# Optimization experiments

Hardware: AMD Instinct MI355X
Metric: run time of the kernel (lower is better)

Reference implementation:

```python
import jax, jax.numpy as jnp
import numpy as np

D_MODEL = 512
N_HEADS = 8
EDGE_FEAT_DIM = 4
NUM_GRAPHS = 64
NODES_PER_GRAPH = 128
N_NODES = NUM_GRAPHS * NODES_PER_GRAPH          # 8192
EDGES_PER_GRAPH = 4096                           # avg degree 32
N_EDGES = NUM_GRAPHS * EDGES_PER_GRAPH           # 262144


def setup_inputs() -> dict:
    key = jax.random.key(0)
    ks = jax.random.split(key, 12)
    s = 0.02
    x = jax.random.normal(ks[0], (N_NODES, D_MODEL), jnp.float32)
    # edges constrained within their graph (block-diagonal structure)
    g_of_e = jnp.arange(N_EDGES, dtype=jnp.int32) // EDGES_PER_GRAPH
    src = g_of_e * NODES_PER_GRAPH + jax.random.randint(ks[1], (N_EDGES,), 0, NODES_PER_GRAPH, jnp.int32)
    dst = g_of_e * NODES_PER_GRAPH + jax.random.randint(ks[2], (N_EDGES,), 0, NODES_PER_GRAPH, jnp.int32)
    edge_index = jnp.stack([src, dst]).astype(jnp.int32)
    edge_attr = jax.random.normal(ks[3], (N_EDGES, EDGE_FEAT_DIM), jnp.float32)
    batch = jnp.repeat(jnp.arange(NUM_GRAPHS, dtype=jnp.int32), NODES_PER_GRAPH)
    # projection weights (in,out) convention: y = x @ W + b
    Wq = jax.random.normal(ks[4], (D_MODEL, D_MODEL), jnp.float32) * s
    Wk = jax.random.normal(ks[5], (D_MODEL, D_MODEL), jnp.float32) * s
    Wv = jax.random.normal(ks[6], (D_MODEL, D_MODEL), jnp.float32) * s
    Wo = jax.random.normal(ks[7], (D_MODEL, D_MODEL), jnp.float32) * s
    bq = jnp.zeros((D_MODEL,), jnp.float32)
    bk = jnp.zeros((D_MODEL,), jnp.float32)
    bv = jnp.zeros((D_MODEL,), jnp.float32)
    bo = jnp.zeros((D_MODEL,), jnp.float32)
    # edge bias MLP: edge_feat_dim -> d_model -> n_heads
    W1 = jax.random.normal(ks[8], (EDGE_FEAT_DIM, D_MODEL), jnp.float32) * s
    b1 = jnp.zeros((D_MODEL,), jnp.float32)
    W2 = jax.random.normal(ks[9], (D_MODEL, N_HEADS), jnp.float32) * s
    b2 = jnp.zeros((N_HEADS,), jnp.float32)
    return {"x": x, "edge_index": edge_index, "edge_attr": edge_attr, "batch": batch,
            "n_g": NODES_PER_GRAPH,
            "Wq": Wq, "bq": bq, "Wk": Wk, "bk": bk, "Wv": Wv, "bv": bv,
            "Wo": Wo, "bo": bo, "W1": W1, "b1": b1, "W2": W2, "b2": b2}


def reference(x, edge_index, edge_attr, batch, n_g, Wq, bq, Wk, bk, Wv, bv, Wo, bo, W1, b1, W2, b2):
    # batch is contiguous equal-size blocks of n_g nodes per graph, so the
    # per-graph Python loop of the original collapses to a batched (G, n_g)
    # block-diagonal attention. Dropout is identity (eval / p used only in train).
    N, d_model = x.shape
    H = W2.shape[1]
    d_k = d_model // H
    G = N // n_g
    scale = 1.0 / float(np.sqrt(d_k))

    Q = (x @ Wq + bq).reshape(G, n_g, H, d_k)
    K = (x @ Wk + bk).reshape(G, n_g, H, d_k)
    V = (x @ Wv + bv).reshape(G, n_g, H, d_k)

    # (G, i, j, h) dense per-graph scores
    scores = jnp.einsum('gihd,gjhd->gijh', Q, K) * scale

    # edge bias: MLP(edge_attr) -> (E, H), scattered at (graph, local_src, local_dst)
    bias = jax.nn.relu(edge_attr @ W1 + b1) @ W2 + b2
    ge = edge_index[0] // n_g
    ls = edge_index[0] % n_g
    ld = edge_index[1] % n_g
    scores = scores.at[ge, ls, ld].add(bias)

    attn = jax.nn.softmax(scores, axis=2)  # softmax over j (keys), matches dim=1 of (i,j,h)
    out = jnp.einsum('gijh,gjhd->gihd', attn, V).reshape(N, d_model)
    return out @ Wo + bo
```

## Files before the change

kernel.cpp:

```cpp
#include <hip/hip_runtime.h>
#include <hip/hip_bf16.h>

#define E_TOTAL 262144
#define NG      128
#define GRAPHS  64
#define NHEADS  8
#define DKH     64
#define DMODEL  512
#define NNODES  8192

typedef __bf16 bf16x8 __attribute__((ext_vector_type(8)));
typedef float  f32x4  __attribute__((ext_vector_type(4)));
typedef short  s16x4  __attribute__((ext_vector_type(4)));
typedef unsigned short u16x8 __attribute__((ext_vector_type(8)));

typedef __attribute__((address_space(3))) char lds_char;
typedef const __attribute__((address_space(1))) char glb_char;

__device__ inline __hip_bfloat16 f2hbf(float f) { return __float2bfloat16(f); }
__device__ inline unsigned short f2u16(float f) {
    return __builtin_bit_cast(unsigned short, __float2bfloat16(f));
}
__device__ inline __bf16 f2bf(float f) {
    return __builtin_bit_cast(__bf16, f2u16(f));
}
__device__ inline bf16x8 cvt8(float4 lo, float4 hi) {
    bf16x8 o;
    o[0] = f2bf(lo.x); o[1] = f2bf(lo.y); o[2] = f2bf(lo.z); o[3] = f2bf(lo.w);
    o[4] = f2bf(hi.x); o[5] = f2bf(hi.y); o[6] = f2bf(hi.z); o[7] = f2bf(hi.w);
    return o;
}

__global__ __launch_bounds__(256) void prep_kernel(
    const float* __restrict__ Wq, const float* __restrict__ Wk,
    const float* __restrict__ Wv, const float* __restrict__ Wo,
    const float* __restrict__ W1, const float* __restrict__ b1,
    const float* __restrict__ W2, const float* __restrict__ b2,
    __hip_bfloat16* __restrict__ wqkvt, __hip_bfloat16* __restrict__ wot,
    __hip_bfloat16* __restrict__ w1fragt, float* __restrict__ b1f,
    __hip_bfloat16* __restrict__ w2at, float* __restrict__ b2f)
{
    int blk = blockIdx.x, tid = threadIdx.x;
    if (blk < 256) {
        __shared__ __align__(16) __hip_bfloat16 tile[64][65];
        const float* src;
        __hip_bfloat16* dstT;
        int n0, k0, nb;
        if (blk < 192) {
            int nt = blk % 24, ktile = blk / 24;
            n0 = nt * 64; k0 = ktile * 64;
            if (n0 < 512)       { src = Wq; nb = n0; }
            else if (n0 < 1024) { src = Wk; nb = n0 - 512; }
            else                { src = Wv; nb = n0 - 1024; }
            dstT = wqkvt;
        } else {
            int t = blk - 192;
            n0 = (t % 8) * 64; k0 = (t / 8) * 64; nb = n0;
            src = Wo; dstT = wot;
        }
        #pragma unroll
        for (int i = 0; i < 16; ++i) {
            int idx = tid + i * 256;
            int kr = idx >> 6, nc = idx & 63;
            tile[kr][nc] = f2hbf(src[(size_t)(k0 + kr) * 512 + nb + nc]);
        }
        __syncthreads();
        #pragma unroll
        for (int i = 0; i < 16; ++i) {
            int idx = tid + i * 256;
            int nr = idx >> 6, kc = idx & 63;
            dstT[(size_t)(n0 + nr) * 512 + k0 + kc] = tile[kc][nr];
        }
    } else {
        __hip_bfloat16 z = f2hbf(0.f);
        for (int n = tid; n < 512; n += 256) {
            #pragma unroll
            for (int j = 0; j < 4; ++j) w1fragt[n * 8 + j] = f2hbf(W1[(size_t)j * 512 + n]);
            #pragma unroll
            for (int j = 4; j < 8; ++j) w1fragt[n * 8 + j] = z;
        }
        for (int i = tid; i < 512; i += 256) b1f[i] = b1[i];
        for (int i = tid; i < 32 * 64 * 4; i += 256) {
            int t = i >> 8, lane = (i >> 2) & 63, j = i & 3;
            int q = lane >> 4, l = lane & 15;
            w2at[i] = (l < 8) ? f2hbf(W2[(size_t)(16 * t + 4 * q + j) * 8 + l]) : z;
        }
        if (tid < 8) b2f[tid] = b2[tid];
    }
}

__device__ __forceinline__ void gemm0_body(
    const float* __restrict__ A, const __hip_bfloat16* __restrict__ BT,
    int row0, int col0,
    const float* __restrict__ bq, const float* __restrict__ bk,
    const float* __restrict__ bv,
    __hip_bfloat16* __restrict__ qkv, __hip_bfloat16* __restrict__ vt,
    __hip_bfloat16* As, __hip_bfloat16* Bs)
{
    const int K = 512;
    int tid = threadIdx.x;
    int lane = tid & 63, quad = lane >> 4, l16 = lane & 15;
    int wave = tid >> 6, wi = wave >> 1, wj = wave & 1;

    f32x4 acc[2][4];
    #pragma unroll
    for (int a = 0; a < 2; a++)
        #pragma unroll
        for (int b = 0; b < 4; b++)
            #pragma unroll
            for (int r = 0; r < 4; r++) acc[a][b][r] = 0.f;

    const float* Ag = A + (size_t)(row0 + (tid >> 2)) * K + (tid & 3) * 8;
    const __hip_bfloat16* Bg0 = BT + (size_t)(col0 + (tid >> 2)) * K + (tid & 3) * 8;
    const __hip_bfloat16* Bg1 = Bg0 + (size_t)64 * K;
    char* BsB = (char*)Bs;
    int lidx = tid * 8;

    for (int kt = 0; kt < K / 32; ++kt) {
        float4 a0l = *(const float4*)(Ag + kt * 32);
        float4 a0h = *(const float4*)(Ag + kt * 32 + 4);
        __syncthreads();
        __builtin_amdgcn_global_load_lds((glb_char*)(Bg0 + kt * 32), (lds_char*)(BsB + tid * 16), 16, 0, 0);
        __builtin_amdgcn_global_load_lds((glb_char*)(Bg1 + kt * 32), (lds_char*)(BsB + 4096 + tid * 16), 16, 0, 0);
        *(bf16x8*)&As[lidx] = cvt8(a0l, a0h);
        __syncthreads();
        bf16x8 af[2], bfr[4];
        #pragma unroll
        for (int t = 0; t < 2; t++)
            af[t] = *(const bf16x8*)&As[(wi * 32 + t * 16 + l16) * 32 + quad * 8];
        #pragma unroll
        for (int t = 0; t < 4; t++)
            bfr[t] = *(const bf16x8*)&Bs[(wj * 64 + t * 16 + l16) * 32 + quad * 8];
        #pragma unroll
        for (int ti = 0; ti < 2; ti++)
            #pragma unroll
            for (int tj = 0; tj < 4; tj++)
                acc[ti][tj] = __builtin_amdgcn_mfma_f32_16x16x32_bf16(af[ti], bfr[tj], acc[ti][tj], 0, 0, 0);
    }

    #pragma unroll
    for (int ti = 0; ti < 2; ti++)
        #pragma unroll
        for (int tj = 0; tj < 4; tj++) {
            int c = col0 + wj * 64 + tj * 16 + l16;
            #pragma unroll
            for (int r = 0; r < 4; r++) {
                int rw = row0 + wi * 32 + ti * 16 + quad * 4 + r;
                float v = acc[ti][tj][r];
                if (c < 1024) {
                    v += (c < 512) ? bq[c] : bk[c - 512];
                    qkv[(size_t)rw * 1536 + c] = f2hbf(v);
                } else {
                    v += bv[c - 1024];
                    int g = rw >> 7, i = rw & 127, hh = (c - 1024) >> 6, d = (c - 1024) & 63;
                    vt[(((size_t)(g * 8 + hh)) * 64 + d) * 128 + i] = f2hbf(v);
                }
            }
        }
}

__device__ __forceinline__ void edge_body(
    int eblk,
    const float* __restrict__ ea,
    const __hip_bfloat16* __restrict__ w1fragt, const float* __restrict__ b1f,
    const __hip_bfloat16* __restrict__ w2at, const float* __restrict__ b2f,
    float* __restrict__ biasE)
{
    int tid = threadIdx.x, wave = tid >> 6, lane = tid & 63;
    int quad = lane >> 4, l16 = lane & 15;
    int eb = eblk * 256 + wave * 64;

    bf16x8 eaf[4] = {};
    if (quad == 0) {
        #pragma unroll
        for (int gg = 0; gg < 4; ++gg) {
            float4 e4 = *(const float4*)(ea + (size_t)(eb + gg * 16 + l16) * 4);
            eaf[gg][0] = f2bf(e4.x); eaf[gg][1] = f2bf(e4.y);
            eaf[gg][2] = f2bf(e4.z); eaf[gg][3] = f2bf(e4.w);
        }
    }

    f32x4 c2[4];
    #pragma unroll
    for (int gg = 0; gg < 4; ++gg)
        #pragma unroll
        for (int r = 0; r < 4; ++r) c2[gg][r] = 0.f;

    #pragma unroll 4
    for (int t = 0; t < 32; ++t) {
        bf16x8 a1 = *(const bf16x8*)(w1fragt + ((size_t)t * 16 + l16) * 8);
        float4 b14 = *(const float4*)(b1f + t * 16 + quad * 4);
        s16x4 a2 = *(const s16x4*)(w2at + ((size_t)t * 64 + lane) * 4);
        #pragma unroll
        for (int gg = 0; gg < 4; ++gg) {
            f32x4 c1 = {0.f, 0.f, 0.f, 0.f};
            c1 = __builtin_amdgcn_mfma_f32_16x16x32_bf16(a1, eaf[gg], c1, 0, 0, 0);
            s16x4 hfrag;
            hfrag[0] = (short)f2u16(fmaxf(c1[0] + b14.x, 0.f));
            hfrag[1] = (short)f2u16(fmaxf(c1[1] + b14.y, 0.f));
            hfrag[2] = (short)f2u16(fmaxf(c1[2] + b14.z, 0.f));
            hfrag[3] = (short)f2u16(fmaxf(c1[3] + b14.w, 0.f));
            c2[gg] = __builtin_amdgcn_mfma_f32_16x16x16bf16_1k(a2, hfrag, c2[gg], 0, 0, 0);
        }
    }
    if (quad < 2) {
        #pragma unroll
        for (int gg = 0; gg < 4; ++gg) {
            #pragma unroll
            for (int r = 0; r < 4; ++r) {
                int hh = quad * 4 + r;
                biasE[(size_t)hh * E_TOTAL + eb + gg * 16 + l16] = c2[gg][r] + b2f[hh];
            }
        }
    }
}

__global__ __launch_bounds__(256) void mega_kernel(
    const float* __restrict__ A, const __hip_bfloat16* __restrict__ BT,
    const float* __restrict__ bq, const float* __restrict__ bk,
    const float* __restrict__ bv,
    __hip_bfloat16* __restrict__ qkv, __hip_bfloat16* __restrict__ vt,
    const float* __restrict__ ea,
    const __hip_bfloat16* __restrict__ w1fragt, const float* __restrict__ b1f,
    const __hip_bfloat16* __restrict__ w2at, const float* __restrict__ b2f,
    float* __restrict__ biasE)
{
    __shared__ __align__(16) __hip_bfloat16 As[64 * 32];
    __shared__ __align__(16) __hip_bfloat16 Bs[128 * 32];
    int blk = blockIdx.x;
    if (blk < 1536) {
        gemm0_body(A, BT, (blk & 127) * 64, (blk >> 7) * 128,
                   bq, bk, bv, qkv, vt, As, Bs);
    } else {
        edge_body(blk - 1536, ea, w1fragt, b1f, w2at, b2f, biasE);
    }
}

__global__ __launch_bounds__(256) void gemm1_kernel(
    const __hip_bfloat16* __restrict__ A, const __hip_bfloat16* __restrict__ BT,
    const float* __restrict__ bo, float* __restrict__ out)
{
    const int K = 512;
    __shared__ __align__(16) __hip_bfloat16 As[128 * 32];
    __shared__ __align__(16) __hip_bfloat16 Bs[64 * 32];
    int tid = threadIdx.x;
    int lane = tid & 63, quad = lane >> 4, l16 = lane & 15;
    int wave = tid >> 6, wi = wave >> 1, wj = wave & 1;
    int row0 = blockIdx.x * 128, col0 = blockIdx.y * 64;

    f32x4 acc[4][2];
    #pragma unroll
    for (int a = 0; a < 4; a++)
        #pragma unroll
        for (int b = 0; b < 2; b++)
            #pragma unroll
            for (int r = 0; r < 4; r++) acc[a][b][r] = 0.f;

    const __hip_bfloat16* Ag0 = A + (size_t)(row0 + (tid >> 2)) * K + (tid & 3) * 8;
    const __hip_bfloat16* Ag1 = Ag0 + (size_t)64 * K;
    const __hip_bfloat16* Bg  = BT + (size_t)(col0 + (tid >> 2)) * K + (tid & 3) * 8;
    char* AsB = (char*)As;
    char* BsB = (char*)Bs;

    for (int kt = 0; kt < K / 32; ++kt) {
        __syncthreads();
        __builtin_amdgcn_global_load_lds((glb_char*)(Ag0 + kt * 32), (lds_char*)(AsB + tid * 16), 16, 0, 0);
        __builtin_amdgcn_global_load_lds((glb_char*)(Ag1 + kt * 32), (lds_char*)(AsB + 4096 + tid * 16), 16, 0, 0);
        __builtin_amdgcn_global_load_lds((glb_char*)(Bg + kt * 32), (lds_char*)(BsB + tid * 16), 16, 0, 0);
        __syncthreads();
        bf16x8 af[4], bfr[2];
        #pragma unroll
        for (int t = 0; t < 4; t++)
            af[t] = *(const bf16x8*)&As[(wi * 64 + t * 16 + l16) * 32 + quad * 8];
        #pragma unroll
        for (int t = 0; t < 2; t++)
            bfr[t] = *(const bf16x8*)&Bs[(wj * 32 + t * 16 + l16) * 32 + quad * 8];
        #pragma unroll
        for (int ti = 0; ti < 4; ti++)
            #pragma unroll
            for (int tj = 0; tj < 2; tj++)
                acc[ti][tj] = __builtin_amdgcn_mfma_f32_16x16x32_bf16(af[ti], bfr[tj], acc[ti][tj], 0, 0, 0);
    }

    #pragma unroll
    for (int ti = 0; ti < 4; ti++)
        #pragma unroll
        for (int tj = 0; tj < 2; tj++) {
            int c = col0 + wj * 32 + tj * 16 + l16;
            #pragma unroll
            for (int r = 0; r < 4; r++) {
                int rw = row0 + wi * 64 + ti * 16 + quad * 4 + r;
                out[(size_t)rw * 512 + c] = acc[ti][tj][r] + bo[c];
            }
        }
}

#define SS 132
__global__ __launch_bounds__(256) void attn_kernel(
    const __hip_bfloat16* __restrict__ qkv,
    const __hip_bfloat16* __restrict__ vt,
    const float* __restrict__ biasE,
    const int* __restrict__ eidx,
    __hip_bfloat16* __restrict__ O)
{
    __shared__ __align__(16) float S[128 * SS];
    int blk = blockIdx.x, g = blk & 63, h = blk >> 6;
    int tid = threadIdx.x, wave = tid >> 6, lane = tid & 63;
    int quad = lane >> 4, l16 = lane & 15;

    int   sa[16];
    float bv[16];
    #pragma unroll
    for (int u = 0; u < 16; ++u) {
        int idx = g * 4096 + tid + u * 256;
        int ls = eidx[idx] & 127;
        int ld = eidx[E_TOTAL + idx] & 127;
        sa[u] = ls * SS + ld;
        bv[u] = biasE[(size_t)h * E_TOTAL + idx];
    }

    const __hip_bfloat16* qbase = qkv + (size_t)(g * 128) * 1536 + h * 64;
    const __hip_bfloat16* kbase = qbase + 512;

    f32x4 acc[2][8];
    #pragma unroll
    for (int t = 0; t < 2; t++)
        #pragma unroll
        for (int j = 0; j < 8; j++)
            #pragma unroll
            for (int r = 0; r < 4; r++) acc[t][j][r] = 0.f;

    #pragma unroll
    for (int k0 = 0; k0 < 64; k0 += 32) {
        bf16x8 af[2];
        #pragma unroll
        for (int t = 0; t < 2; t++) {
            int m = wave * 32 + t * 16 + l16;
            af[t] = *(const bf16x8*)(qbase + (size_t)m * 1536 + k0 + quad * 8);
        }
        #pragma unroll
        for (int tj = 0; tj < 8; tj++) {
            int n = tj * 16 + l16;
            bf16x8 bfr = *(const bf16x8*)(kbase + (size_t)n * 1536 + k0 + quad * 8);
            #pragma unroll
            for (int t = 0; t < 2; t++)
                acc[t][tj] = __builtin_amdgcn_mfma_f32_16x16x32_bf16(af[t], bfr, acc[t][tj], 0, 0, 0);
        }
    }
    #pragma unroll
    for (int t = 0; t < 2; t++)
        #pragma unroll
        for (int tj = 0; tj < 8; tj++)
            #pragma unroll
            for (int r = 0; r < 4; r++) {
                int i = wave * 32 + t * 16 + quad * 4 + r;
                int j = tj * 16 + l16;
                S[i * SS + j] = acc[t][tj][r] * 0.125f;
            }
    __syncthreads();

    #pragma unroll
    for (int u = 0; u < 16; ++u)
        atomicAdd(&S[sa[u]], bv[u]);
    __syncthreads();

    #pragma unroll 4
    for (int r = wave * 32; r < wave * 32 + 32; ++r) {
        float2 v = *(const float2*)&S[r * SS + 2 * lane];
        float m = fmaxf(v.x, v.y);
        #pragma unroll
        for (int off = 32; off > 0; off >>= 1) m = fmaxf(m, __shfl_xor(m, off));
        float e0 = __expf(v.x - m), e1 = __expf(v.y - m);
        float s = e0 + e1;
        #pragma unroll
        for (int off = 32; off > 0; off >>= 1) s += __shfl_xor(s, off);
        float inv = 1.0f / s;
        float2 o; o.x = e0 * inv; o.y = e1 * inv;
        *(float2*)&S[r * SS + 2 * lane] = o;
    }
    __syncthreads();

    f32x4 oacc[2][4];
    #pragma unroll
    for (int t = 0; t < 2; t++)
        #pragma unroll
        for (int j = 0; j < 4; j++)
            #pragma unroll
            for (int r = 0; r < 4; r++) oacc[t][j][r] = 0.f;

    const __hip_bfloat16* vbase = vt + (size_t)(g * 8 + h) * 64 * 128;
    #pragma unroll
    for (int k0 = 0; k0 < 128; k0 += 32) {
        bf16x8 af[2];
        #pragma unroll
        for (int t = 0; t < 2; t++) {
            int m = wave * 32 + t * 16 + l16;
            const float* p = &S[m * SS + k0 + quad * 8];
            f32x4 xa = *(const f32x4*)p;
            f32x4 xb = *(const f32x4*)(p + 4);
            bf16x8 a;
            a[0] = f2bf(xa[0]); a[1] = f2bf(xa[1]); a[2] = f2bf(xa[2]); a[3] = f2bf(xa[3]);
            a[4] = f2bf(xb[0]); a[5] = f2bf(xb[1]); a[6] = f2bf(xb[2]); a[7] = f2bf(xb[3]);
            af[t] = a;
        }
        #pragma unroll
        for (int tj = 0; tj < 4; tj++) {
            int d = tj * 16 + l16;
            bf16x8 bfr = *(const bf16x8*)(vbase + (size_t)d * 128 + k0 + quad * 8);
            #pragma unroll
            for (int t = 0; t < 2; t++)
                oacc[t][tj] = __builtin_amdgcn_mfma_f32_16x16x32_bf16(af[t], bfr, oacc[t][tj], 0, 0, 0);
        }
    }
    #pragma unroll
    for (int t = 0; t < 2; t++)
        #pragma unroll
        for (int tj = 0; tj < 4; tj++)
            #pragma unroll
            for (int r = 0; r < 4; r++) {
                int i = wave * 32 + t * 16 + quad * 4 + r;
                int d = tj * 16 + l16;
                O[(size_t)(g * 128 + i) * 512 + h * 64 + d] = f2hbf(oacc[t][tj][r]);
            }
}

#define WS_WQKVT 0x0
#define WS_WOT   0x180000
#define WS_W1FR  0x200000
#define WS_B1F   0x202000
#define WS_W2AT  0x202800
#define WS_B2F   0x206800
#define WS_QKV   0xA10000
#define WS_VT    0x2210000
#define WS_BIASE 0x2A10000
#define WS_O     0x3210000

extern "C" void kernel_launch(void* const* d_in, const int* in_sizes, int n_in,
                              void* d_out, int out_size, void* d_ws, size_t ws_size,
                              hipStream_t stream) {
    const float* x    = (const float*)d_in[0];
    const int*   eidx = (const int*)d_in[1];
    const float* ea   = (const float*)d_in[2];
    const float* Wq = (const float*)d_in[5];
    const float* bq = (const float*)d_in[6];
    const float* Wk = (const float*)d_in[7];
    const float* bk = (const float*)d_in[8];
    const float* Wv = (const float*)d_in[9];
    const float* bv = (const float*)d_in[10];
    const float* Wo = (const float*)d_in[11];
    const float* bo = (const float*)d_in[12];
    const float* W1 = (const float*)d_in[13];
    const float* b1 = (const float*)d_in[14];
    const float* W2 = (const float*)d_in[15];
    const float* b2 = (const float*)d_in[16];

    char* ws = (char*)d_ws;
    __hip_bfloat16* wqkvt   = (__hip_bfloat16*)(ws + WS_WQKVT);
    __hip_bfloat16* wot     = (__hip_bfloat16*)(ws + WS_WOT);
    __hip_bfloat16* w1fragt = (__hip_bfloat16*)(ws + WS_W1FR);
    float* b1f   = (float*)(ws + WS_B1F);
    __hip_bfloat16* w2at    = (__hip_bfloat16*)(ws + WS_W2AT);
    float* b2f   = (float*)(ws + WS_B2F);
    __hip_bfloat16* qkv = (__hip_bfloat16*)(ws + WS_QKV);
    __hip_bfloat16* vt  = (__hip_bfloat16*)(ws + WS_VT);
    float* biasE = (float*)(ws + WS_BIASE);
    __hip_bfloat16* O   = (__hip_bfloat16*)(ws + WS_O);

    prep_kernel<<<257, 256, 0, stream>>>(Wq, Wk, Wv, Wo, W1, b1, W2, b2,
                                         wqkvt, wot, w1fragt, b1f, w2at, b2f);
    mega_kernel<<<1536 + E_TOTAL / 256, 256, 0, stream>>>(
        x, wqkvt, bq, bk, bv, qkv, vt,
        ea, w1fragt, b1f, w2at, b2f, biasE);
    attn_kernel<<<GRAPHS * NHEADS, 256, 0, stream>>>(qkv, vt, biasE, eidx, O);
    gemm1_kernel<<<dim3(NNODES / 128, 512 / 64), 256, 0, stream>>>(
        O, wot, bo, (float*)d_out);
}
```

Before: 209.6 us.

## Double-buffer GEMM LDS tiles, pre-convert x to bf16, shrink edge MLP MFMA

Result: slower. 217.7 us (+3.8%).

```diff
diff --git a/kernel.cpp b/kernel.cpp
--- a/kernel.cpp
+++ b/kernel.cpp
@@ -36,6 +36,7 @@
     const float* __restrict__ Wv, const float* __restrict__ Wo,
     const float* __restrict__ W1, const float* __restrict__ b1,
     const float* __restrict__ W2, const float* __restrict__ b2,
+    const float* __restrict__ x, __hip_bfloat16* __restrict__ xbf,
     __hip_bfloat16* __restrict__ wqkvt, __hip_bfloat16* __restrict__ wot,
     __hip_bfloat16* __restrict__ w1fragt, float* __restrict__ b1f,
     __hip_bfloat16* __restrict__ w2at, float* __restrict__ b2f)
@@ -71,13 +72,11 @@
             int nr = idx >> 6, kc = idx & 63;
             dstT[(size_t)(n0 + nr) * 512 + k0 + kc] = tile[kc][nr];
         }
-    } else {
+    } else if (blk == 256) {
         __hip_bfloat16 z = f2hbf(0.f);
         for (int n = tid; n < 512; n += 256) {
             #pragma unroll
-            for (int j = 0; j < 4; ++j) w1fragt[n * 8 + j] = f2hbf(W1[(size_t)j * 512 + n]);
-            #pragma unroll
-            for (int j = 4; j < 8; ++j) w1fragt[n * 8 + j] = z;
+            for (int j = 0; j < 4; ++j) w1fragt[n * 4 + j] = f2hbf(W1[(size_t)j * 512 + n]);
         }
         for (int i = tid; i < 512; i += 256) b1f[i] = b1[i];
         for (int i = tid; i < 32 * 64 * 4; i += 256) {
@@ -86,16 +85,21 @@
             w2at[i] = (l < 8) ? f2hbf(W2[(size_t)(16 * t + 4 * q + j) * 8 + l]) : z;
         }
         if (tid < 8) b2f[tid] = b2[tid];
+    } else {
+        int base = (blk - 257) * 2048 + tid * 8;
+        float4 lo = *(const float4*)(x + base);
+        float4 hi = *(const float4*)(x + base + 4);
+        *(bf16x8*)(xbf + base) = cvt8(lo, hi);
     }
 }
 
 __device__ __forceinline__ void gemm0_body(
-    const float* __restrict__ A, const __hip_bfloat16* __restrict__ BT,
+    const __hip_bfloat16* __restrict__ A, const __hip_bfloat16* __restrict__ BT,
     int row0, int col0,
     const float* __restrict__ bq, const float* __restrict__ bk,
     const float* __restrict__ bv,
     __hip_bfloat16* __restrict__ qkv, __hip_bfloat16* __restrict__ vt,
-    __hip_bfloat16* As, __hip_bfloat16* Bs)
+    __hip_bfloat16* __restrict__ As, __hip_bfloat16* __restrict__ Bs)
 {
     const int K = 512;
     int tid = threadIdx.x;
@@ -110,32 +114,43 @@
             #pragma unroll
             for (int r = 0; r < 4; r++) acc[a][b][r] = 0.f;
 
-    const float* Ag = A + (size_t)(row0 + (tid >> 2)) * K + (tid & 3) * 8;
+    const __hip_bfloat16* Ag  = A + (size_t)(row0 + (tid >> 2)) * K + (tid & 3) * 8;
     const __hip_bfloat16* Bg0 = BT + (size_t)(col0 + (tid >> 2)) * K + (tid & 3) * 8;
     const __hip_bfloat16* Bg1 = Bg0 + (size_t)64 * K;
+    char* AsB = (char*)As;
     char* BsB = (char*)Bs;
-    int lidx = tid * 8;
-
-    for (int kt = 0; kt < K / 32; ++kt) {
-        float4 a0l = *(const float4*)(Ag + kt * 32);
-        float4 a0h = *(const float4*)(Ag + kt * 32 + 4);
-        __syncthreads();
-        __builtin_amdgcn_global_load_lds((glb_char*)(Bg0 + kt * 32), (lds_char*)(BsB + tid * 16), 16, 0, 0);
-        __builtin_amdgcn_global_load_lds((glb_char*)(Bg1 + kt * 32), (lds_char*)(BsB + 4096 + tid * 16), 16, 0, 0);
-        *(bf16x8*)&As[lidx] = cvt8(a0l, a0h);
-        __syncthreads();
+
+    __builtin_amdgcn_global_load_lds((glb_char*)Ag,  (lds_char*)(AsB + tid * 16), 16, 0, 0);
+    __builtin_amdgcn_global_load_lds((glb_char*)Bg0, (lds_char*)(BsB + tid * 16), 16, 0, 0);
+    __builtin_amdgcn_global_load_lds((glb_char*)Bg1, (lds_char*)(BsB + 4096 + tid * 16), 16, 0, 0);
+    __syncthreads();
+
+    #pragma unroll 2
+    for (int kt = 0; kt < 16; ++kt) {
+        int cur = kt & 1, nxt = cur ^ 1;
+        if (kt < 15) {
+            __builtin_amdgcn_global_load_lds((glb_char*)(Ag + (kt + 1) * 32),
+                (lds_char*)(AsB + nxt * 4096 + tid * 16), 16, 0, 0);
+            __builtin_amdgcn_global_load_lds((glb_char*)(Bg0 + (kt + 1) * 32),
+                (lds_char*)(BsB + nxt * 8192 + tid * 16), 16, 0, 0);
+            __builtin_amdgcn_global_load_lds((glb_char*)(Bg1 + (kt + 1) * 32),
+                (lds_char*)(BsB + nxt * 8192 + 4096 + tid * 16), 16, 0, 0);
+        }
+        const __hip_bfloat16* Asc = As + cur * 2048;
+        const __hip_bfloat16* Bsc = Bs + cur * 4096;
         bf16x8 af[2], bfr[4];
         #pragma unroll
         for (int t = 0; t < 2; t++)
-            af[t] = *(const bf16x8*)&As[(wi * 32 + t * 16 + l16) * 32 + quad * 8];
+            af[t] = *(const bf16x8*)&Asc[(wi * 32 + t * 16 + l16) * 32 + quad * 8];
         #pragma unroll
         for (int t = 0; t < 4; t++)
-            bfr[t] = *(const bf16x8*)&Bs[(wj * 64 + t * 16 + l16) * 32 + quad * 8];
+            bfr[t] = *(const bf16x8*)&Bsc[(wj * 64 + t * 16 + l16) * 32 + quad * 8];
         #pragma unroll
         for (int ti = 0; ti < 2; ti++)
             #pragma unroll
             for (int tj = 0; tj < 4; tj++)
                 acc[ti][tj] = __builtin_amdgcn_mfma_f32_16x16x32_bf16(af[ti], bfr[tj], acc[ti][tj], 0, 0, 0);
+        __syncthreads();
     }
 
     #pragma unroll
@@ -170,13 +185,13 @@
     int quad = lane >> 4, l16 = lane & 15;
     int eb = eblk * 256 + wave * 64;
 
-    bf16x8 eaf[4] = {};
+    s16x4 eaf[4] = {};
     if (quad == 0) {
         #pragma unroll
         for (int gg = 0; gg < 4; ++gg) {
             float4 e4 = *(const float4*)(ea + (size_t)(eb + gg * 16 + l16) * 4);
-            eaf[gg][0] = f2bf(e4.x); eaf[gg][1] = f2bf(e4.y);
-            eaf[gg][2] = f2bf(e4.z); eaf[gg][3] = f2bf(e4.w);
+            eaf[gg][0] = (short)f2u16(e4.x); eaf[gg][1] = (short)f2u16(e4.y);
+            eaf[gg][2] = (short)f2u16(e4.z); eaf[gg][3] = (short)f2u16(e4.w);
         }
     }
 
@@ -188,13 +203,13 @@
 
     #pragma unroll 4
     for (int t = 0; t < 32; ++t) {
-        bf16x8 a1 = *(const bf16x8*)(w1fragt + ((size_t)t * 16 + l16) * 8);
+        s16x4 a1 = *(const s16x4*)(w1fragt + ((size_t)t * 16 + l16) * 4);
         float4 b14 = *(const float4*)(b1f + t * 16 + quad * 4);
         s16x4 a2 = *(const s16x4*)(w2at + ((size_t)t * 64 + lane) * 4);
         #pragma unroll
         for (int gg = 0; gg < 4; ++gg) {
             f32x4 c1 = {0.f, 0.f, 0.f, 0.f};
-            c1 = __builtin_amdgcn_mfma_f32_16x16x32_bf16(a1, eaf[gg], c1, 0, 0, 0);
+            c1 = __builtin_amdgcn_mfma_f32_16x16x16bf16_1k(a1, eaf[gg], c1, 0, 0, 0);
             s16x4 hfrag;
             hfrag[0] = (short)f2u16(fmaxf(c1[0] + b14.x, 0.f));
             hfrag[1] = (short)f2u16(fmaxf(c1[1] + b14.y, 0.f));
@@ -216,7 +231,7 @@
 }
 
 __global__ __launch_bounds__(256) void mega_kernel(
-    const float* __restrict__ A, const __hip_bfloat16* __restrict__ BT,
+    const __hip_bfloat16* __restrict__ A, const __hip_bfloat16* __restrict__ BT,
     const float* __restrict__ bq, const float* __restrict__ bk,
     const float* __restrict__ bv,
     __hip_bfloat16* __restrict__ qkv, __hip_bfloat16* __restrict__ vt,
@@ -225,8 +240,8 @@
     const __hip_bfloat16* __restrict__ w2at, const float* __restrict__ b2f,
     float* __restrict__ biasE)
 {
-    __shared__ __align__(16) __hip_bfloat16 As[64 * 32];
-    __shared__ __align__(16) __hip_bfloat16 Bs[128 * 32];
+    __shared__ __align__(16) __hip_bfloat16 As[2 * 64 * 32];
+    __shared__ __align__(16) __hip_bfloat16 Bs[2 * 128 * 32];
     int blk = blockIdx.x;
     if (blk < 1536) {
         gemm0_body(A, BT, (blk & 127) * 64, (blk >> 7) * 128,
@@ -241,8 +256,8 @@
     const float* __restrict__ bo, float* __restrict__ out)
 {
     const int K = 512;
-    __shared__ __align__(16) __hip_bfloat16 As[128 * 32];
-    __shared__ __align__(16) __hip_bfloat16 Bs[64 * 32];
+    __shared__ __align__(16) __hip_bfloat16 As[2 * 128 * 32];
+    __shared__ __align__(16) __hip_bfloat16 Bs[2 * 64 * 32];
     int tid = threadIdx.x;
     int lane = tid & 63, quad = lane >> 4, l16 = lane & 15;
     int wave = tid >> 6, wi = wave >> 1, wj = wave & 1;
@@ -262,24 +277,37 @@
     char* AsB = (char*)As;
     char* BsB = (char*)Bs;
 
-    for (int kt = 0; kt < K / 32; ++kt) {
-        __syncthreads();
-        __builtin_amdgcn_global_load_lds((glb_char*)(Ag0 + kt * 32), (lds_char*)(AsB + tid * 16), 16, 0, 0);
-        __builtin_amdgcn_global_load_lds((glb_char*)(Ag1 + kt * 32), (lds_char*)(AsB + 4096 + tid * 16), 16, 0, 0);
-        __builtin_amdgcn_global_load_lds((glb_char*)(Bg + kt * 32), (lds_char*)(BsB + tid * 16), 16, 0, 0);
-        __syncthreads();
+    __builtin_amdgcn_global_load_lds((glb_char*)Ag0, (lds_char*)(AsB + tid * 16), 16, 0, 0);
+    __builtin_amdgcn_global_load_lds((glb_char*)Ag1, (lds_char*)(AsB + 4096 + tid * 16), 16, 0, 0);
+    __builtin_amdgcn_global_load_lds((glb_char*)Bg,  (lds_char*)(BsB + tid * 16), 16, 0, 0);
+    __syncthreads();
+
+    #pragma unroll 2
+    for (int kt = 0; kt < 16; ++kt) {
+        int cur = kt & 1, nxt = cur ^ 1;
+        if (kt < 15) {
+            __builtin_amdgcn_global_load_lds((glb_char*)(Ag0 + (kt + 1) * 32),
+                (lds_char*)(AsB + nxt * 8192 + tid * 16), 16, 0, 0);
+            __builtin_amdgcn_global_load_lds((glb_char*)(Ag1 + (kt + 1) * 32),
+                (lds_char*)(AsB + nxt * 8192 + 4096 + tid * 16), 16, 0, 0);
+            __builtin_amdgcn_global_load_lds((glb_char*)(Bg + (kt + 1) * 32),
+                (lds_char*)(BsB + nxt * 4096 + tid * 16), 16, 0, 0);
+        }
+        const __hip_bfloat16* Asc = As + cur * 4096;
+        const __hip_bfloat16* Bsc = Bs + cur * 2048;
         bf16x8 af[4], bfr[2];
         #pragma unroll
         for (int t = 0; t < 4; t++)
-            af[t] = *(const bf16x8*)&As[(wi * 64 + t * 16 + l16) * 32 + quad * 8];
+            af[t] = *(const bf16x8*)&Asc[(wi * 64 + t * 16 + l16) * 32 + quad * 8];
         #pragma unroll
         for (int t = 0; t < 2; t++)
-            bfr[t] = *(const bf16x8*)&Bs[(wj * 32 + t * 16 + l16) * 32 + quad * 8];
+            bfr[t] = *(const bf16x8*)&Bsc[(wj * 32 + t * 16 + l16) * 32 + quad * 8];
         #pragma unroll
         for (int ti = 0; ti < 4; ti++)
             #pragma unroll
             for (int tj = 0; tj < 2; tj++)
                 acc[ti][tj] = __builtin_amdgcn_mfma_f32_16x16x32_bf16(af[ti], bfr[tj], acc[ti][tj], 0, 0, 0);
+        __syncthreads();
     }
 
     #pragma unroll
@@ -434,6 +462,7 @@
 #define WS_VT    0x2210000
 #define WS_BIASE 0x2A10000
 #define WS_O     0x3210000
+#define WS_XBF   WS_O
 
 extern "C" void kernel_launch(void* const* d_in, const int* in_sizes, int n_in,
                               void* d_out, int out_size, void* d_ws, size_t ws_size,
@@ -465,11 +494,13 @@
     __hip_bfloat16* vt  = (__hip_bfloat16*)(ws + WS_VT);
     float* biasE = (float*)(ws + WS_BIASE);
     __hip_bfloat16* O   = (__hip_bfloat16*)(ws + WS_O);
-
-    prep_kernel<<<257, 256, 0, stream>>>(Wq, Wk, Wv, Wo, W1, b1, W2, b2,
-                                         wqkvt, wot, w1fragt, b1f, w2at, b2f);
+    __hip_bfloat16* xbf = (__hip_bfloat16*)(ws + WS_XBF);
+
+    prep_kernel<<<257 + 2048, 256, 0, stream>>>(Wq, Wk, Wv, Wo, W1, b1, W2, b2,
+                                                x, xbf,
+                                                wqkvt, wot, w1fragt, b1f, w2at, b2f);
     mega_kernel<<<1536 + E_TOTAL / 256, 256, 0, stream>>>(
-        x, wqkvt, bq, bk, bv, qkv, vt,
+        xbf, wqkvt, bq, bk, bv, qkv, vt,
         ea, w1fragt, b1f, w2at, b2f, biasE);
     attn_kernel<<<GRAPHS * NHEADS, 256, 0, stream>>>(qkv, vt, biasE, eidx, O);
     gemm1_kernel<<<dim3(NNODES / 128, 512 / 64), 256, 0, stream>>>(
```
